# Optimization experiments

Measured on AMD Instinct MI355X. Metric: run time of the kernel, lower is better.

The kernel has to match this reference:

```python
import jax, jax.numpy as jnp
import numpy as np

B, T, OBS, ACT, H, S = 512, 64, 1024, 32, 1024, 64


def setup_inputs() -> dict:
    key = jax.random.key(0)
    ks = jax.random.split(key, 16)
    w = lambda k, shape: 0.02 * jax.random.normal(k, shape, jnp.float32)
    return {
        "obs": jax.random.normal(ks[0], (B, T, OBS), jnp.float32),
        "action": jax.random.normal(ks[1], (B, T, ACT), jnp.float32),
        "eps": jax.random.normal(ks[2], (B, T, S), jnp.float32),
        # obs encoder: Linear(OBS->H) + ReLU
        "W_enc": w(ks[3], (H, OBS)), "b_enc": jnp.zeros((H,), jnp.float32),
        # GRUCell(stoch+action -> H), torch gate order: r, z, n
        "W_ih": w(ks[4], (3 * H, S + ACT)), "W_hh": w(ks[5], (3 * H, H)),
        "b_ih": jnp.zeros((3 * H,), jnp.float32), "b_hh": jnp.zeros((3 * H,), jnp.float32),
        # prior: Linear(H -> 2S); posterior: Linear(2H -> 2S)
        "W_prior": w(ks[6], (2 * S, H)), "b_prior": jnp.zeros((2 * S,), jnp.float32),
        "W_post": w(ks[7], (2 * S, 2 * H)), "b_post": jnp.zeros((2 * S,), jnp.float32),
        # decoder: Linear(H+S -> H) ReLU Linear(H -> OBS)
        "W_dec1": w(ks[8], (H, H + S)), "b_dec1": jnp.zeros((H,), jnp.float32),
        "W_dec2": w(ks[9], (OBS, H)), "b_dec2": jnp.zeros((OBS,), jnp.float32),
        # reward / done heads: Linear(H+S -> 1)
        "W_rew": w(ks[10], (1, H + S)), "b_rew": jnp.zeros((1,), jnp.float32),
        "W_done": w(ks[11], (1, H + S)), "b_done": jnp.zeros((1,), jnp.float32),
    }


def _stats(x):
    mean, raw_std = jnp.split(x, 2, axis=-1)
    return mean, jax.nn.softplus(raw_std) + 1e-4


def reference(obs, action, eps, W_enc, b_enc, W_ih, W_hh, b_ih, b_hh,
              W_prior, b_prior, W_post, b_post, W_dec1, b_dec1, W_dec2, b_dec2,
              W_rew, b_rew, W_done, b_done):
    batch = obs.shape[0]
    hid = W_hh.shape[1]
    sdim = eps.shape[-1]
    # obs encoder is per-step independent -> batch it over time up front
    emb_all = jax.nn.relu(jnp.einsum('bto,ho->bth', obs, W_enc) + b_enc)

    def step(carry, xs):
        deter, stoch = carry
        a_t, emb_t, eps_t = xs
        # torch GRUCell
        x = jnp.concatenate([stoch, a_t], axis=-1)
        gi = x @ W_ih.T + b_ih
        gh = deter @ W_hh.T + b_hh
        i_r, i_z, i_n = jnp.split(gi, 3, axis=-1)
        h_r, h_z, h_n = jnp.split(gh, 3, axis=-1)
        r = jax.nn.sigmoid(i_r + h_r)
        z = jax.nn.sigmoid(i_z + h_z)
        n = jnp.tanh(i_n + r * h_n)
        deter = (1.0 - z) * n + z * deter
        # prior / posterior stats
        p_mean, p_std = _stats(deter @ W_prior.T + b_prior)
        q_mean, q_std = _stats(jnp.concatenate([deter, emb_t], axis=-1) @ W_post.T + b_post)
        stoch = q_mean + eps_t * q_std  # reparam sample
        feat = jnp.concatenate([deter, stoch], axis=-1)
        pred = jax.nn.relu(feat @ W_dec1.T + b_dec1) @ W_dec2.T + b_dec2
        rew = feat @ W_rew.T + b_rew
        done = feat @ W_done.T + b_done
        kl = jnp.log(p_std / q_std) + (q_std ** 2 + (q_mean - p_mean) ** 2) / (2.0 * p_std ** 2) - 0.5
        return (deter, stoch), (pred, rew, done, kl.mean(axis=-1, keepdims=True))

    init = (jnp.zeros((batch, hid), obs.dtype), jnp.zeros((batch, sdim), obs.dtype))
    xs = (jnp.swapaxes(action, 0, 1), jnp.swapaxes(emb_all, 0, 1), jnp.swapaxes(eps, 0, 1))
    _, (preds, rews, dones, kls) = jax.lax.scan(step, init, xs)
    pred = jnp.swapaxes(preds, 0, 1)    # [B,T,OBS]
    reward = jnp.swapaxes(rews, 0, 1)   # [B,T,1]
    done = jnp.swapaxes(dones, 0, 1)    # [B,T,1]
    kl = kls.mean()
    return pred, reward, done, kl
```

## Files before the change

kernel.cpp:

```cpp
#include <hip/hip_runtime.h>
#include <stdint.h>

#define BB 512
#define TT 64
#define OBSD 1024
#define ACTD 32
#define HD 1024
#define SD 64
#define BT (BB*TT)
#define G3 (3*HD)
#define STRD ((long)TT*HD)

typedef unsigned int uint32;
typedef unsigned long long ull;
typedef unsigned short u16;
typedef __attribute__((ext_vector_type(8))) short bf16x8;
typedef __attribute__((ext_vector_type(4))) float f32x4;

__device__ __forceinline__ float bf2f(u16 v){ uint32_t u = ((uint32_t)v)<<16; return __builtin_bit_cast(float,u); }
__device__ __forceinline__ u16 f2bf(float f){ uint32_t u = __builtin_bit_cast(uint32_t,f); uint32_t r = (u + 0x7FFFu + ((u>>16)&1u))>>16; return (u16)r; }
__device__ __forceinline__ float sigm(float x){ return 1.f/(1.f+expf(-x)); }
#define MFMA __builtin_amdgcn_mfma_f32_16x16x32_bf16

__device__ __forceinline__ void gload16(const u16* g, u16* l){
  __builtin_amdgcn_global_load_lds(
      (const __attribute__((address_space(1))) u16*)g,
      (__attribute__((address_space(3))) u16*)l, 16, 0, 0);
}

__global__ void cvt_kernel(const float* __restrict__ in, u16* __restrict__ out, long n){
  long i = (long)blockIdx.x*blockDim.x + threadIdx.x;
  long st = (long)gridDim.x*blockDim.x;
  for (; i<n; i+=st) out[i] = f2bf(in[i]);
}

struct GemmP {
  const u16* a0; const u16* a1; const u16* a2;
  const u16* b0; const u16* b1; const u16* b2;
  long lda0, lda1, lda2, ldb0, ldb1, ldb2;
  int kc0, kc1, kc2, kcPerZ;
  float* cf; u16* cb;
  long ldc, ldcb, zstride;
  const float* bias0; const float* bias1;
  int relu;
};

template<int BM,int BN>
__global__ __launch_bounds__(256) void gemm_bf16(GemmP p){
  __shared__ __align__(16) u16 sAB[2][(BM+BN)*32];
  const int m0 = blockIdx.y*BM, n0 = blockIdx.x*BN;
  const int tid = threadIdx.x, lane = tid&63, wave = tid>>6;
  const int wm = (wave>>1)*(BM/2), wn = (wave&1)*(BN/2);
  constexpr int FM = BM/32, FN = BN/32;
  f32x4 acc[FM][FN] = {};
  const int cbeg = blockIdx.z*p.kcPerZ;
  int cend = cbeg + p.kcPerZ; if (cend > p.kc2) cend = p.kc2;
  const int kg = lane>>4, lr = lane&15;
  const int srow = lane>>2, scol = (lane&3)*8;

  auto STAGE = [&](int buf, int c){
    const u16* ap; const u16* bp; long lda, ldb; int kofs;
    if (c < p.kc0){ ap=p.a0; bp=p.b0; lda=p.lda0; ldb=p.ldb0; kofs=c*32; }
    else if (c < p.kc1){ ap=p.a1; bp=p.b1; lda=p.lda1; ldb=p.ldb1; kofs=(c-p.kc0)*32; }
    else { ap=p.a2; bp=p.b2; lda=p.lda2; ldb=p.ldb2; kofs=(c-p.kc1)*32; }
    u16* base = sAB[buf];
    #pragma unroll
    for (int it=0; it<BM/64; ++it){
      int row = it*64 + wave*16 + srow;
      gload16(ap + (long)(m0+row)*lda + kofs + scol,
              base + (it*64 + wave*16)*32);
    }
    #pragma unroll
    for (int it=0; it<BN/64; ++it){
      int row = it*64 + wave*16 + srow;
      gload16(bp + (long)(n0+row)*ldb + kofs + scol,
              base + BM*32 + (it*64 + wave*16)*32);
    }
  };

  STAGE(0, cbeg);
  for (int c=cbeg;c<cend;++c){
    const int cur = (c-cbeg)&1;
    asm volatile("s_waitcnt vmcnt(0)" ::: "memory");
    __syncthreads();
    if (c+1 < cend) STAGE(cur^1, c+1);
    const u16* sA = sAB[cur];
    const u16* sB = sAB[cur] + BM*32;
    bf16x8 af[FM], bfv[FN];
    #pragma unroll
    for (int i=0;i<FM;++i) af[i] = *(const bf16x8*)&sA[(wm+i*16+lr)*32 + kg*8];
    #pragma unroll
    for (int j=0;j<FN;++j) bfv[j] = *(const bf16x8*)&sB[(wn+j*16+lr)*32 + kg*8];
    #pragma unroll
    for (int i=0;i<FM;++i)
      #pragma unroll
      for (int j=0;j<FN;++j)
        acc[i][j] = MFMA(af[i], bfv[j], acc[i][j], 0,0,0);
    __syncthreads();
  }
  const bool partial = (gridDim.z > 1);
  float* cf = p.cf ? (p.cf + (partial ? (long)blockIdx.z*p.zstride : 0)) : nullptr;
  #pragma unroll
  for (int i=0;i<FM;++i){
    #pragma unroll
    for (int j=0;j<FN;++j){
      const int gr0 = m0 + wm + i*16 + kg*4;
      const int gc = n0 + wn + j*16 + lr;
      float bias = 0.f;
      if (!partial){
        if (p.bias0) bias += p.bias0[gc];
        if (p.bias1) bias += p.bias1[gc];
      }
      #pragma unroll
      for (int r=0;r<4;++r){
        float v = acc[i][j][r] + bias;
        if (p.relu) v = fmaxf(v, 0.f);
        const long row = gr0 + r;
        if (cf) cf[row*p.ldc + gc] = v;
        if (p.cb) p.cb[row*p.ldcb + gc] = f2bf(v);
      }
    }
  }
}

struct ScanArgs {
  const u16* act; const u16* Wih; const u16* Whh;
  const float* b_ih; const float* b_hh;
  const u16* Wpos; const float* qemb; const float* eps;
  u16* det; u16* sto; float* qm; float* qs;
  uint32* slots; const u16* zeroB;
};

__device__ __forceinline__ void gsync_g(uint32* slots, int m, int n, uint32 val){
  asm volatile("s_waitcnt vmcnt(0)" ::: "memory");
  __syncthreads();
  if (threadIdx.x == 0)
    __hip_atomic_store(&slots[m*64 + n], val, __ATOMIC_RELAXED, __HIP_MEMORY_SCOPE_AGENT);
  if (threadIdx.x < 32){
    while (__hip_atomic_load(&slots[m*64 + threadIdx.x], __ATOMIC_RELAXED,
                             __HIP_MEMORY_SCOPE_AGENT) < val)
      __builtin_amdgcn_s_sleep(2);
  }
  __syncthreads();
}


__global__ __launch_bounds__(256, 1) void scan_kernel(ScanArgs A){
  __shared__ __align__(16) u16 lds[(64+96)*128];
  u16* sA = lds; u16* sB = lds + 64*128;
  float* pf = (float*)lds;
  const int bid = blockIdx.x;
  const int tid = threadIdx.x, lane = tid&63, wave = tid>>6;
  const int lr = lane&15, kg = lane>>4;
  const int n = bid&31, m = bid>>5;
  const int m0 = m*64, h0 = n*32;
  const int wrow = (wave&1)*32, wcol = (wave>>1)*16;

  const int srow = tid>>4;
  const int scu  = (tid&15)*8;
  const int scuS = ((tid&15) ^ srow)*8;

  long whhb[6], wihb[6];
  #pragma unroll
  for (int i=0;i<6;++i){
    int br = srow + i*16;
    int gate = br>>5, hr = br&31;
    whhb[i] = (long)(gate*HD + h0 + hr)*HD + scu;
    wihb[i] = (long)(gate*HD + h0 + hr)*96 + scu;
  }

  const int h4 = h0 + wcol + kg*4;
  float bir[4], bhr[4], biz[4], bhz[4], bin[4], bhn[4];
  #pragma unroll
  for (int r=0;r<4;++r){
    bir[r]=A.b_ih[h4+r];      bhr[r]=A.b_hh[h4+r];
    biz[r]=A.b_ih[HD+h4+r];   bhz[r]=A.b_hh[HD+h4+r];
    bin[r]=A.b_ih[2*HD+h4+r]; bhn[r]=A.b_hh[2*HD+h4+r];
  }

  const int pj = n & 3, prt = n >> 2;

  float dreg[2][4] = {{0.f,0.f,0.f,0.f},{0.f,0.f,0.f,0.f}};
  const bf16x8 zerov = {};

  bf16x8 paQ[3][4], pb[6];
  auto loadA = [&](int tt, int g, bf16x8 (&dst)[4]){
    if (g < 8){
      if (tt > 0){
        const u16* s = A.det + (long)(tt-1)*HD + g*128 + scu;
        #pragma unroll
        for (int j=0;j<4;++j) dst[j] = *(const bf16x8*)(s + (long)(m0+srow+16*j)*STRD);
      } else { dst[0]=zerov; dst[1]=zerov; dst[2]=zerov; dst[3]=zerov; }
    } else {
      if (scu < 64){
        if (tt > 0){
          #pragma unroll
          for (int j=0;j<4;++j)
            dst[j] = *(const bf16x8*)(A.sto + (long)(m0+srow+16*j)*((long)TT*SD) + (long)(tt-1)*SD + scu);
        } else { dst[0]=zerov; dst[1]=zerov; dst[2]=zerov; dst[3]=zerov; }
      } else if (scu < 96){
        #pragma unroll
        for (int j=0;j<4;++j)
          dst[j] = *(const bf16x8*)(A.act + (long)(m0+srow+16*j)*((long)TT*ACTD) + (long)tt*ACTD + (scu-64));
      } else { dst[0]=zerov; dst[1]=zerov; dst[2]=zerov; dst[3]=zerov; }
    }
  };
  auto loadB = [&](int g){
    if (g < 8){
      #pragma unroll
      for (int i=0;i<6;++i) pb[i] = *(const bf16x8*)(A.Whh + whhb[i] + g*128);
    } else {
      #pragma unroll
      for (int i=0;i<6;++i) pb[i] = (scu < 96) ? *(const bf16x8*)(A.Wih + wihb[i]) : zerov;
    }
  };

  loadA(0, 0, paQ[0]); loadA(0, 1, paQ[1]); loadA(0, 2, paQ[2]); loadB(0);

  for (int t=0; t<TT; ++t){
    f32x4 aR[2]={}, aZ[2]={}, aNd[2]={}, aNx[2]={};
    #pragma unroll
    for (int g=0; g<9; ++g){
      __syncthreads();
      #pragma unroll
      for (int j=0;j<4;++j) *(bf16x8*)&sA[(srow+16*j)*128 + scuS] = paQ[g%3][j];
      #pragma unroll
      for (int i=0;i<6;++i) *(bf16x8*)&sB[(srow+16*i)*128 + scuS] = pb[i];
      if (g < 8) loadB(g+1);
      if (g+3 <= 8) loadA(t, g+3, paQ[(g+3)%3]);
      __syncthreads();
      #pragma unroll
      for (int k=0;k<4;++k){
        const int sl = ((k*4+kg) ^ lr)*8;
        bf16x8 a0v = *(const bf16x8*)&sA[(wrow+lr)*128 + sl];
        bf16x8 a1v = *(const bf16x8*)&sA[(wrow+16+lr)*128 + sl];
        bf16x8 b0 = *(const bf16x8*)&sB[(wcol+lr)*128 + sl];
        bf16x8 b1 = *(const bf16x8*)&sB[(32+wcol+lr)*128 + sl];
        bf16x8 b2 = *(const bf16x8*)&sB[(64+wcol+lr)*128 + sl];
        aR[0] = MFMA(b0,a0v,aR[0],0,0,0); aR[1] = MFMA(b0,a1v,aR[1],0,0,0);
        aZ[0] = MFMA(b1,a0v,aZ[0],0,0,0); aZ[1] = MFMA(b1,a1v,aZ[1],0,0,0);
        if (g<8){ aNd[0] = MFMA(b2,a0v,aNd[0],0,0,0); aNd[1] = MFMA(b2,a1v,aNd[1],0,0,0); }
        else    { aNx[0] = MFMA(b2,a0v,aNx[0],0,0,0); aNx[1] = MFMA(b2,a1v,aNx[1],0,0,0); }
      }
    }
    #pragma unroll
    for (int rf=0;rf<2;++rf){
      const long brow = m0 + wrow + rf*16 + lr;
      u16 pk[4];
      #pragma unroll
      for (int r=0;r<4;++r){
        float rr = sigm(aR[rf][r]+bir[r]+bhr[r]);
        float z  = sigm(aZ[rf][r]+biz[r]+bhz[r]);
        float nn = tanhf(aNx[rf][r]+bin[r] + rr*(aNd[rf][r]+bhn[r]));
        float d = (1.f - z)*nn + z*dreg[rf][r];
        dreg[rf][r] = d;
        pk[r] = f2bf(d);
      }
      ull pv; __builtin_memcpy(&pv, pk, 8);
      __hip_atomic_store((ull*)(A.det + brow*STRD + (long)t*HD + h4), pv,
                         __ATOMIC_RELAXED, __HIP_MEMORY_SCOPE_AGENT);
    }
    gsync_g(A.slots, m, n, (uint32)(2*t+1));

    {
      f32x4 accM = {}, accS = {};
      const int k0 = wave*256;
      const u16* arow = A.det + (long)(m0 + prt*8 + (lr&7))*STRD + (long)t*HD + k0 + kg*8;
      const u16* bm = A.Wpos + (long)(pj*16 + lr)*(2*HD) + k0 + kg*8;
      const u16* bs = A.Wpos + (long)(64 + pj*16 + lr)*(2*HD) + k0 + kg*8;
      #pragma unroll
      for (int kk=0; kk<8; ++kk){
        bf16x8 af = *(const bf16x8*)(arow + kk*32);
        accM = MFMA(af, *(const bf16x8*)(bm + kk*32), accM, 0,0,0);
        accS = MFMA(af, *(const bf16x8*)(bs + kk*32), accS, 0,0,0);
      }
      #pragma unroll
      for (int r=0;r<4;++r){
        int rowt = kg*4 + r;
        pf[wave*512 + rowt*16 + lr]       = accM[r];
        pf[wave*512 + 256 + rowt*16 + lr] = accS[r];
      }
      __syncthreads();
      if (tid < 64){
        const int row = tid>>3;
        const int s2 = (tid&7)*2;
        const long grow = m0 + prt*8 + row;
        const float* qe = A.qemb + grow*((long)TT*128) + (long)t*128;
        const float* ep = A.eps  + grow*((long)TT*SD) + (long)t*SD;
        u16 spk[2];
        #pragma unroll
        for (int i=0;i<2;++i){
          int sl = s2 + i, sg = pj*16 + sl;
          float mean = pf[row*16+sl] + pf[512+row*16+sl] + pf[1024+row*16+sl] + pf[1536+row*16+sl];
          float rsv  = pf[256+row*16+sl] + pf[768+row*16+sl] + pf[1280+row*16+sl] + pf[1792+row*16+sl];
          mean += qe[sg];
          rsv  += qe[64+sg];
          float sp = fmaxf(rsv,0.f) + log1pf(expf(-fabsf(rsv)));
          float qs_ = sp + 1e-4f;
          float st = mean + ep[sg]*qs_;
          A.qm[grow*((long)TT*SD) + (long)t*SD + sg] = mean;
          A.qs[grow*((long)TT*SD) + (long)t*SD + sg] = qs_;
          spk[i] = f2bf(st);
        }
        uint32 pv; __builtin_memcpy(&pv, spk, 4);
        __hip_atomic_store((uint32*)(A.sto + grow*((long)TT*SD) + (long)t*SD + pj*16 + s2), pv,
                           __ATOMIC_RELAXED, __HIP_MEMORY_SCOPE_AGENT);
      }
      __syncthreads();
    }
    if (t+1 < TT){
      loadA(t+1, 0, paQ[0]);
      loadA(t+1, 1, paQ[1]);
      loadA(t+1, 2, paQ[2]);
      loadB(0);
    }
    gsync_g(A.slots, m, n, (uint32)(2*t+2));
  }
}

__global__ __launch_bounds__(256) void gru_step(
    const u16* __restrict__ sto_prev, long ssto,
    const u16* __restrict__ act_t,
    const u16* __restrict__ det_prev, long sdet,
    const u16* __restrict__ Wih, const u16* __restrict__ Whh,
    const float* __restrict__ b_ih, const float* __restrict__ b_hh,
    float* __restrict__ deterF, u16* __restrict__ det_bf_t){
  constexpr int SA = 40;
  __shared__ u16 sA[32*SA];
  __shared__ u16 sB[96*SA];
  const int id = blockIdx.x;
  const int n = (id&7) + ((id>>7)<<3);
  const int m = (id>>3)&15;
  const int m0 = m*32, h0 = n*32;
  const int tid = threadIdx.x, lane = tid&63, wave = tid>>6;
  const int wm = wave>>1, wn = wave&1;
  const int lr = lane&15, kg = lane>>4;

  f32x4 aR = {}, aZ = {}, aNd = {}, aNx = {};

  auto aAddr = [&](int c, int row, int sc)->const u16*{
    if (c < 32) return det_prev + (long)(m0+row)*sdet + c*32 + sc;
    if (c < 34) return sto_prev + (long)(m0+row)*ssto + (c-32)*32 + sc;
    return act_t + (long)(m0+row)*((long)TT*ACTD) + sc;
  };
  auto bAddr = [&](int c, int l)->const u16*{
    int row = l>>2, sc = (l&3)*8;
    int g = row>>5, hr = row&31;
    if (c < 32) return Whh + (long)(g*1024 + h0 + hr)*HD + c*32 + sc;
    return Wih + (long)(g*1024 + h0 + hr)*(SD+ACTD) + (c-32)*32 + sc;
  };

  bf16x8 rA, rB0, rB1;
  auto loadc = [&](int c){
    rB0 = *(const bf16x8*)bAddr(c, tid);
    if (tid < 128){
      rA  = *(const bf16x8*)aAddr(c, tid>>2, (tid&3)*8);
      rB1 = *(const bf16x8*)bAddr(c, 256+tid);
    }
  };

  loadc(0);
  for (int c=0; c<35; ++c){
    *(bf16x8*)&sB[(tid>>2)*SA + (tid&3)*8] = rB0;
    if (tid < 128){
      *(bf16x8*)&sA[(tid>>2)*SA + (tid&3)*8] = rA;
      int l = 256+tid;
      *(bf16x8*)&sB[(l>>2)*SA + (l&3)*8] = rB1;
    }
    if (c < 34) loadc(c+1);
    __syncthreads();
    bf16x8 af = *(const bf16x8*)&sA[(wm*16+lr)*SA + kg*8];
    bf16x8 b0 = *(const bf16x8*)&sB[(     wn*16+lr)*SA + kg*8];
    bf16x8 b1 = *(const bf16x8*)&sB[(32 + wn*16+lr)*SA + kg*8];
    bf16x8 b2 = *(const bf16x8*)&sB[(64 + wn*16+lr)*SA + kg*8];
    aR = MFMA(af,b0,aR,0,0,0);
    aZ = MFMA(af,b1,aZ,0,0,0);
    if (c < 32) aNd = MFMA(af,b2,aNd,0,0,0);
    else        aNx = MFMA(af,b2,aNx,0,0,0);
    __syncthreads();
  }

  const int col = h0 + wn*16 + lr;
  const float bir = b_ih[col],      bhr = b_hh[col];
  const float biz = b_ih[col+HD],   bhz = b_hh[col+HD];
  const float bin = b_ih[col+2*HD], bhn = b_hh[col+2*HD];
  #pragma unroll
  for (int reg=0; reg<4; ++reg){
    const int row = m0 + wm*16 + kg*4 + reg;
    float r = sigm(aR[reg] + bir + bhr);
    float z = sigm(aZ[reg] + biz + bhz);
    float nn = tanhf(aNx[reg] + bin + r*(aNd[reg] + bhn));
    const long fidx = (long)row*HD + col;
    float d = (1.f - z)*nn + z*deterF[fidx];
    deterF[fidx] = d;
    det_bf_t[(long)row*STRD + col] = f2bf(d);
  }
}

__global__ __launch_bounds__(256) void post_step(
    const u16* __restrict__ det_t,
    const u16* __restrict__ Wpos,
    const float* __restrict__ qemb_t,
    const float* __restrict__ eps_t,
    float* __restrict__ qm_t, float* __restrict__ qs_t, u16* __restrict__ sto_out){
  constexpr int SA = 40;
  __shared__ u16 sA4[4*16*SA];
  __shared__ u16 sB4[4*128*SA];
  const int m0 = blockIdx.x*16;
  const int tid = threadIdx.x, lane = tid&63, w = tid>>6;
  const int lr = lane&15, kg = lane>>4;

  f32x4 acc[8] = {};
  bf16x8 rA, rB[8];
  auto loadIter = [&](int i){
    #pragma unroll
    for (int rnd=0; rnd<8; ++rnd){
      int l = rnd*256 + tid;
      int q = l>>9, row = (l>>2)&127, sc = (l&3)*8;
      rB[rnd] = *(const bf16x8*)(Wpos + (long)row*(2*HD) + (q*8+i)*32 + sc);
    }
    { int q = tid>>6, row = (tid>>2)&15, sc = (tid&3)*8;
      rA = *(const bf16x8*)(det_t + (long)(m0+row)*STRD + (q*8+i)*32 + sc); }
  };

  loadIter(0);
  for (int i=0; i<8; ++i){
    #pragma unroll
    for (int rnd=0; rnd<8; ++rnd){
      int l = rnd*256 + tid;
      int q = l>>9, row = (l>>2)&127, sc = (l&3)*8;
      *(bf16x8*)&sB4[q*128*SA + row*SA + sc] = rB[rnd];
    }
    { int q = tid>>6, row = (tid>>2)&15, sc = (tid&3)*8;
      *(bf16x8*)&sA4[q*16*SA + row*SA + sc] = rA; }
    if (i < 7) loadIter(i+1);
    __syncthreads();
    bf16x8 af = *(const bf16x8*)&sA4[w*16*SA + lr*SA + kg*8];
    #pragma unroll
    for (int j=0; j<8; ++j){
      bf16x8 bf = *(const bf16x8*)&sB4[w*128*SA + (j*16+lr)*SA + kg*8];
      acc[j] = MFMA(af, bf, acc[j], 0,0,0);
    }
    __syncthreads();
  }

  float* pf = (float*)sB4;
  #pragma unroll
  for (int j=0; j<8; ++j)
    #pragma unroll
    for (int reg=0; reg<4; ++reg)
      pf[w*2048 + (kg*4+reg)*128 + j*16+lr] = acc[j][reg];
  __syncthreads();

  #pragma unroll
  for (int i=0; i<4; ++i){
    int p = tid + i*256;
    int row = p>>6, s = p&63;
    int b = m0 + row;
    float mval = pf[row*128+s]      + pf[2048+row*128+s]      + pf[4096+row*128+s]      + pf[6144+row*128+s];
    float rsv  = pf[row*128+64+s]   + pf[2048+row*128+64+s]   + pf[4096+row*128+64+s]   + pf[6144+row*128+64+s];
    mval += qemb_t[(long)b*((long)TT*128) + s];
    rsv  += qemb_t[(long)b*((long)TT*128) + 64 + s];
    float sp = fmaxf(rsv,0.f) + log1pf(expf(-fabsf(rsv)));
    float qsv = sp + 1e-4f;
    float e = eps_t[(long)b*((long)TT*SD) + s];
    float st = mval + e*qsv;
    qm_t[(long)b*((long)TT*SD) + s] = mval;
    qs_t[(long)b*((long)TT*SD) + s] = qsv;
    sto_out[(long)b*((long)TT*SD) + s] = f2bf(st);
  }
}

__global__ void kl_kernel(const float* __restrict__ pbuf, const float* __restrict__ qm,
                          const float* __restrict__ qs, float* __restrict__ klrows){
  int m = blockIdx.x*4 + (threadIdx.x>>6);
  int s = threadIdx.x & 63;
  float pm   = pbuf[(long)m*128 + s];
  float praw = pbuf[(long)m*128 + 64 + s];
  float ps = fmaxf(praw,0.f) + log1pf(expf(-fabsf(praw))) + 1e-4f;
  float qmv = qm[(long)m*64+s], qsv = qs[(long)m*64+s];
  float d = qmv - pm;
  float kl = logf(ps/qsv) + (qsv*qsv + d*d)/(2.f*ps*ps) - 0.5f;
  #pragma unroll
  for (int off=32; off; off>>=1) kl += __shfl_xor(kl, off);
  if (s==0) klrows[m] = kl*(1.f/64.f);
}

__global__ void kl_reduce(const float* __restrict__ klrows, float* __restrict__ out){
  __shared__ float sm[256];
  float a = 0.f;
  for (int i=threadIdx.x; i<BT; i+=256) a += klrows[i];
  sm[threadIdx.x]=a; __syncthreads();
  for (int off=128; off; off>>=1){ if ((int)threadIdx.x<off) sm[threadIdx.x]+=sm[threadIdx.x+off]; __syncthreads(); }
  if (threadIdx.x==0) out[0] = sm[0] / (float)BT;
}

__global__ void rewdone_kernel(const u16* __restrict__ det, const u16* __restrict__ sto,
    const float* __restrict__ Wr, const float* __restrict__ br,
    const float* __restrict__ Wd, const float* __restrict__ bd,
    float* __restrict__ orew, float* __restrict__ odone){
  int m = blockIdx.x*4 + (threadIdx.x>>6);
  int lane = threadIdx.x & 63;
  float ar=0.f, ad=0.f;
  for (int k=lane; k<HD+SD; k+=64){
    float f = (k<HD) ? bf2f(det[(long)m*HD+k]) : bf2f(sto[(long)m*SD + (k-HD)]);
    ar = fmaf(f, Wr[k], ar); ad = fmaf(f, Wd[k], ad);
  }
  #pragma unroll
  for (int off=32; off; off>>=1){ ar += __shfl_xor(ar, off); ad += __shfl_xor(ad, off); }
  if (lane==0){ orew[m]=ar+br[0]; odone[m]=ad+bd[0]; }
}

static char* carve(char*& base, size_t bytes){
  char* p = base; base += (bytes + 255) & ~(size_t)255; return p;
}

extern "C" void kernel_launch(void* const* d_in, const int* in_sizes, int n_in,
                              void* d_out, int out_size, void* d_ws, size_t ws_size,
                              hipStream_t stream) {
  const float* obs    = (const float*)d_in[0];
  const float* action = (const float*)d_in[1];
  const float* eps    = (const float*)d_in[2];
  const float* W_enc  = (const float*)d_in[3];
  const float* b_enc  = (const float*)d_in[4];
  const float* W_ih   = (const float*)d_in[5];
  const float* W_hh   = (const float*)d_in[6];
  const float* b_ih   = (const float*)d_in[7];
  const float* b_hh   = (const float*)d_in[8];
  const float* W_prior= (const float*)d_in[9];
  const float* b_prior= (const float*)d_in[10];
  const float* W_post = (const float*)d_in[11];
  const float* b_post = (const float*)d_in[12];
  const float* W_dec1 = (const float*)d_in[13];
  const float* b_dec1 = (const float*)d_in[14];
  const float* W_dec2 = (const float*)d_in[15];
  const float* b_dec2 = (const float*)d_in[16];
  const float* W_rew  = (const float*)d_in[17];
  const float* b_rew  = (const float*)d_in[18];
  const float* W_done = (const float*)d_in[19];
  const float* b_done = (const float*)d_in[20];

  char* w = (char*)d_ws;
  u16* obs_bf  = (u16*)carve(w, (size_t)BT*OBSD*2);
  u16* emb_bf  = (u16*)carve(w, (size_t)BT*HD*2);
  u16* det_bf  = (u16*)carve(w, (size_t)BT*HD*2);
  u16* sto_bf  = (u16*)carve(w, (size_t)BT*SD*2);
  u16* act_bf  = (u16*)carve(w, (size_t)BT*ACTD*2);
  u16* Wenc_bf = (u16*)carve(w, (size_t)HD*OBSD*2);
  u16* Wih_bf  = (u16*)carve(w, (size_t)G3*(SD+ACTD)*2);
  u16* Whh_bf  = (u16*)carve(w, (size_t)G3*HD*2);
  u16* Wpri_bf = (u16*)carve(w, (size_t)2*SD*HD*2);
  u16* Wpos_bf = (u16*)carve(w, (size_t)2*SD*2*HD*2);
  u16* Wd1_bf  = (u16*)carve(w, (size_t)HD*(HD+SD)*2);
  u16* Wd2_bf  = (u16*)carve(w, (size_t)OBSD*HD*2);
  u16* zero_bf = (u16*)carve(w, 4096);
  float* deterF = (float*)carve(w, (size_t)BB*HD*4);
  float* qemb   = (float*)carve(w, (size_t)BT*128*4);
  float* qm_all = (float*)carve(w, (size_t)BT*SD*4);
  float* qs_all = (float*)carve(w, (size_t)BT*SD*4);
  float* p_buf  = (float*)carve(w, (size_t)BT*2*SD*4);
  float* klrows = (float*)carve(w, (size_t)BT*4);
  uint32* syncb = (uint32*)carve(w, 8192);
  u16* hid_bf = obs_bf;

  if ((size_t)(w - (char*)d_ws) > ws_size){
    hipMemsetAsync(d_out, 0xFF, 4, stream);
    return;
  }

  auto cvt = [&](const float* in, u16* out, long n){
    cvt_kernel<<<dim3(2048), dim3(256), 0, stream>>>(in, out, n);
  };
  cvt(obs, obs_bf, (long)BT*OBSD);
  cvt(action, act_bf, (long)BT*ACTD);
  cvt(W_enc, Wenc_bf, (long)HD*OBSD);
  cvt(W_ih, Wih_bf, (long)G3*(SD+ACTD));
  cvt(W_hh, Whh_bf, (long)G3*HD);
  cvt(W_prior, Wpri_bf, (long)2*SD*HD);
  cvt(W_post, Wpos_bf, (long)2*SD*2*HD);
  cvt(W_dec1, Wd1_bf, (long)HD*(HD+SD));
  cvt(W_dec2, Wd2_bf, (long)OBSD*HD);
  hipMemsetAsync(zero_bf, 0, 4096, stream);
  hipMemsetAsync(deterF, 0, (size_t)BB*HD*4, stream);
  hipMemsetAsync(syncb, 0, 8192, stream);

  {
    GemmP q{};
    q.a0 = obs_bf;  q.lda0 = OBSD;
    q.b0 = Wenc_bf; q.ldb0 = OBSD;
    q.kc0=q.kc1=q.kc2=32; q.kcPerZ=32;
    q.cb = emb_bf; q.ldcb = HD;
    q.bias0 = b_enc; q.relu = 1;
    gemm_bf16<128,128><<<dim3(HD/128, BT/128, 1), 256, 0, stream>>>(q);
  }
  {
    GemmP q{};
    q.a0 = emb_bf;       q.lda0 = HD;
    q.b0 = Wpos_bf + HD; q.ldb0 = 2*HD;
    q.kc0=q.kc1=q.kc2=32; q.kcPerZ=32;
    q.cf = qemb; q.ldc = 128;
    q.bias0 = b_post;
    gemm_bf16<64,64><<<dim3(128/64, BT/64, 1), 256, 0, stream>>>(q);
  }

  {
    ScanArgs sa;
    sa.act = act_bf; sa.Wih = Wih_bf; sa.Whh = Whh_bf;
    sa.b_ih = b_ih; sa.b_hh = b_hh;
    sa.Wpos = Wpos_bf; sa.qemb = qemb; sa.eps = eps;
    sa.det = det_bf; sa.sto = sto_bf; sa.qm = qm_all; sa.qs = qs_all;
    sa.slots = syncb; sa.zeroB = zero_bf;
    void* kargs[] = { (void*)&sa };
    hipError_t cerr = hipLaunchCooperativeKernel((const void*)scan_kernel,
        dim3(256), dim3(256), kargs, 0, stream);
    if (cerr != hipSuccess){
      for (int t=0; t<TT; ++t){
        const u16* sto_p = (t==0) ? zero_bf : (sto_bf + (long)(t-1)*SD);
        long ssto        = (t==0) ? 0 : (long)TT*SD;
        const u16* det_p = (t==0) ? zero_bf : (det_bf + (long)(t-1)*HD);
        long sdet        = (t==0) ? 0 : STRD;
        gru_step<<<dim3(512), 256, 0, stream>>>(sto_p, ssto, act_bf + (long)t*ACTD,
            det_p, sdet, Wih_bf, Whh_bf, b_ih, b_hh, deterF, det_bf + (long)t*HD);
        post_step<<<dim3(32), 256, 0, stream>>>(det_bf + (long)t*HD, Wpos_bf,
            qemb + (long)t*128, eps + (long)t*SD,
            qm_all + (long)t*SD, qs_all + (long)t*SD, sto_bf + (long)t*SD);
      }
    }
  }

  {
    GemmP q{};
    q.a0 = det_bf;  q.lda0 = HD;
    q.b0 = Wpri_bf; q.ldb0 = HD;
    q.kc0=q.kc1=q.kc2=32; q.kcPerZ=32;
    q.cf = p_buf; q.ldc = 2*SD;
    q.bias0 = b_prior;
    gemm_bf16<64,64><<<dim3(2*SD/64, BT/64, 1), 256, 0, stream>>>(q);
  }
  kl_kernel<<<dim3(BT/4), 256, 0, stream>>>(p_buf, qm_all, qs_all, klrows);
  {
    GemmP q{};
    q.a0 = det_bf; q.lda0 = HD;
    q.a1 = sto_bf; q.lda1 = SD;
    q.b0 = Wd1_bf;      q.ldb0 = HD+SD;
    q.b1 = Wd1_bf + HD; q.ldb1 = HD+SD;
    q.kc0=32; q.kc1=34; q.kc2=34; q.kcPerZ=34;
    q.cb = hid_bf; q.ldcb = HD;
    q.bias0 = b_dec1; q.relu = 1;
    gemm_bf16<128,128><<<dim3(HD/128, BT/128, 1), 256, 0, stream>>>(q);
  }
  {
    GemmP q{};
    q.a0 = hid_bf; q.lda0 = HD;
    q.b0 = Wd2_bf; q.ldb0 = HD;
    q.kc0=q.kc1=q.kc2=32; q.kcPerZ=32;
    q.cf = (float*)d_out; q.ldc = OBSD;
    q.bias0 = b_dec2;
    gemm_bf16<128,128><<<dim3(OBSD/128, BT/128, 1), 256, 0, stream>>>(q);
  }
  rewdone_kernel<<<dim3(BT/4), 256, 0, stream>>>(det_bf, sto_bf, W_rew, b_rew, W_done, b_done,
      (float*)d_out + (long)BT*OBSD, (float*)d_out + (long)BT*OBSD + BT);
  kl_reduce<<<dim3(1), 256, 0, stream>>>(klrows, (float*)d_out + (long)BT*OBSD + 2*BT);
}
```

Before: 1.592 ms.

## Load GRU weight fragments directly into registers, bypassing LDS staging

The recurrent scan kernel now loads W_hh/W_ih B-operand fragments straight from global memory into per-lane MFMA register layout, double-buffered across gate chunks, instead of staging them through shared memory. This removes the LDS writes and reads for the weight tile and shrinks the shared allocation. The full __syncthreads barriers are also replaced by an lgkmcnt wait plus a raw s_barrier, which no longer waits on outstanding global loads. The cost is higher register pressure (two 12-vector fragment buffers) and less coalesced global reads per lane.

```diff
diff --git a/kernel.cpp b/kernel.cpp
--- a/kernel.cpp
+++ b/kernel.cpp
@@ -146,8 +146,8 @@
 
 
 __global__ __launch_bounds__(256, 1) void scan_kernel(ScanArgs A){
-  __shared__ __align__(16) u16 lds[(64+96)*128];
-  u16* sA = lds; u16* sB = lds + 64*128;
+  __shared__ __align__(16) u16 lds[64*128];
+  u16* sA = lds;
   float* pf = (float*)lds;
   const int bid = blockIdx.x;
   const int tid = threadIdx.x, lane = tid&63, wave = tid>>6;
@@ -160,15 +160,6 @@
   const int scu  = (tid&15)*8;
   const int scuS = ((tid&15) ^ srow)*8;
 
-  long whhb[6], wihb[6];
-  #pragma unroll
-  for (int i=0;i<6;++i){
-    int br = srow + i*16;
-    int gate = br>>5, hr = br&31;
-    whhb[i] = (long)(gate*HD + h0 + hr)*HD + scu;
-    wihb[i] = (long)(gate*HD + h0 + hr)*96 + scu;
-  }
-
   const int h4 = h0 + wcol + kg*4;
   float bir[4], bhr[4], biz[4], bhz[4], bin[4], bhn[4];
   #pragma unroll
@@ -183,7 +174,30 @@
   float dreg[2][4] = {{0.f,0.f,0.f,0.f},{0.f,0.f,0.f,0.f}};
   const bf16x8 zerov = {};
 
-  bf16x8 paQ[3][4], pb[6];
+  const long bRowW = (long)(h0 + wcol + lr);
+  bf16x8 bw0[3][4], bw1[3][4];
+  auto loadBfrag = [&](int g, bf16x8 (&dst)[3][4]){
+    if (g < 8){
+      const u16* base = A.Whh + bRowW*HD + g*128 + kg*8;
+      #pragma unroll
+      for (int s=0;s<3;++s){
+        #pragma unroll
+        for (int k=0;k<4;++k)
+          dst[s][k] = *(const bf16x8*)(base + (long)s*((long)HD*HD) + k*32);
+      }
+    } else {
+      const u16* base = A.Wih + bRowW*96 + kg*8;
+      #pragma unroll
+      for (int s=0;s<3;++s){
+        #pragma unroll
+        for (int k=0;k<3;++k)
+          dst[s][k] = *(const bf16x8*)(base + (long)s*((long)HD*96) + k*32);
+        dst[s][3] = zerov;
+      }
+    }
+  };
+
+  bf16x8 paQ[3][4];
   auto loadA = [&](int tt, int g, bf16x8 (&dst)[4]){
     if (g < 8){
       if (tt > 0){
@@ -205,43 +219,37 @@
       } else { dst[0]=zerov; dst[1]=zerov; dst[2]=zerov; dst[3]=zerov; }
     }
   };
-  auto loadB = [&](int g){
-    if (g < 8){
-      #pragma unroll
-      for (int i=0;i<6;++i) pb[i] = *(const bf16x8*)(A.Whh + whhb[i] + g*128);
-    } else {
-      #pragma unroll
-      for (int i=0;i<6;++i) pb[i] = (scu < 96) ? *(const bf16x8*)(A.Wih + wihb[i]) : zerov;
-    }
-  };
-
-  loadA(0, 0, paQ[0]); loadA(0, 1, paQ[1]); loadA(0, 2, paQ[2]); loadB(0);
+
+  f32x4 aR[2], aZ[2], aNd[2], aNx[2];
+  auto mmaG = [&](int g, bf16x8 (&bw)[3][4]){
+    #pragma unroll
+    for (int k=0;k<4;++k){
+      const int sl = ((k*4+kg) ^ lr)*8;
+      bf16x8 a0v = *(const bf16x8*)&sA[(wrow+lr)*128 + sl];
+      bf16x8 a1v = *(const bf16x8*)&sA[(wrow+16+lr)*128 + sl];
+      aR[0] = MFMA(bw[0][k],a0v,aR[0],0,0,0); aR[1] = MFMA(bw[0][k],a1v,aR[1],0,0,0);
+      aZ[0] = MFMA(bw[1][k],a0v,aZ[0],0,0,0); aZ[1] = MFMA(bw[1][k],a1v,aZ[1],0,0,0);
+      if (g<8){ aNd[0] = MFMA(bw[2][k],a0v,aNd[0],0,0,0); aNd[1] = MFMA(bw[2][k],a1v,aNd[1],0,0,0); }
+      else    { aNx[0] = MFMA(bw[2][k],a0v,aNx[0],0,0,0); aNx[1] = MFMA(bw[2][k],a1v,aNx[1],0,0,0); }
+    }
+  };
+
+  loadA(0, 0, paQ[0]); loadA(0, 1, paQ[1]); loadA(0, 2, paQ[2]); loadBfrag(0, bw0);
 
   for (int t=0; t<TT; ++t){
-    f32x4 aR[2]={}, aZ[2]={}, aNd[2]={}, aNx[2]={};
+    #pragma unroll
+    for (int i=0;i<2;++i){ aR[i]=f32x4{}; aZ[i]=f32x4{}; aNd[i]=f32x4{}; aNx[i]=f32x4{}; }
     #pragma unroll
     for (int g=0; g<9; ++g){
-      __syncthreads();
+      asm volatile("s_waitcnt lgkmcnt(0)" ::: "memory");
+      __builtin_amdgcn_s_barrier();
       #pragma unroll
       for (int j=0;j<4;++j) *(bf16x8*)&sA[(srow+16*j)*128 + scuS] = paQ[g%3][j];
-      #pragma unroll
-      for (int i=0;i<6;++i) *(bf16x8*)&sB[(srow+16*i)*128 + scuS] = pb[i];
-      if (g < 8) loadB(g+1);
+      if (g < 8){ if (g&1) loadBfrag(g+1, bw0); else loadBfrag(g+1, bw1); }
       if (g+3 <= 8) loadA(t, g+3, paQ[(g+3)%3]);
-      __syncthreads();
-      #pragma unroll
-      for (int k=0;k<4;++k){
-        const int sl = ((k*4+kg) ^ lr)*8;
-        bf16x8 a0v = *(const bf16x8*)&sA[(wrow+lr)*128 + sl];
-        bf16x8 a1v = *(const bf16x8*)&sA[(wrow+16+lr)*128 + sl];
-        bf16x8 b0 = *(const bf16x8*)&sB[(wcol+lr)*128 + sl];
-        bf16x8 b1 = *(const bf16x8*)&sB[(32+wcol+lr)*128 + sl];
-        bf16x8 b2 = *(const bf16x8*)&sB[(64+wcol+lr)*128 + sl];
-        aR[0] = MFMA(b0,a0v,aR[0],0,0,0); aR[1] = MFMA(b0,a1v,aR[1],0,0,0);
-        aZ[0] = MFMA(b1,a0v,aZ[0],0,0,0); aZ[1] = MFMA(b1,a1v,aZ[1],0,0,0);
-        if (g<8){ aNd[0] = MFMA(b2,a0v,aNd[0],0,0,0); aNd[1] = MFMA(b2,a1v,aNd[1],0,0,0); }
-        else    { aNx[0] = MFMA(b2,a0v,aNx[0],0,0,0); aNx[1] = MFMA(b2,a1v,aNx[1],0,0,0); }
-      }
+      asm volatile("s_waitcnt lgkmcnt(0)" ::: "memory");
+      __builtin_amdgcn_s_barrier();
+      if (g&1) mmaG(g, bw1); else mmaG(g, bw0);
     }
     #pragma unroll
     for (int rf=0;rf<2;++rf){
@@ -312,7 +320,7 @@
       loadA(t+1, 0, paQ[0]);
       loadA(t+1, 1, paQ[1]);
       loadA(t+1, 2, paQ[2]);
-      loadB(0);
+      loadBfrag(0, bw0);
     }
     gsync_g(A.slots, m, n, (uint32)(2*t+2));
   }
```

Result: slower. 2.066 ms (+29.8%).
